# Kernel optimization log

Hardware: AMD Instinct MI355X
Metric: run time of the kernel (lower is better)

The kernel has to match this reference:

```python
import jax, jax.numpy as jnp
import numpy as np

EMBED_DIM = 1024
NUM_HEADS = 16
HEAD_DIM = EMBED_DIM // NUM_HEADS
B, S = 2, 2048


def setup_inputs() -> dict:
    key = jax.random.key(0)
    ks = jax.random.split(key, 11)
    scale = 1.0 / np.sqrt(EMBED_DIM)
    inp = {
        "q": jax.random.normal(ks[0], (B, S, EMBED_DIM), jnp.float32),
        "k": jax.random.normal(ks[1], (B, S, EMBED_DIM), jnp.float32),
        "v": jax.random.normal(ks[2], (B, S, EMBED_DIM), jnp.float32),
        "Wq": jax.random.normal(ks[3], (EMBED_DIM, EMBED_DIM), jnp.float32) * scale,
        "bq": jnp.zeros((EMBED_DIM,), jnp.float32),
        "Wk": jax.random.normal(ks[4], (EMBED_DIM, EMBED_DIM), jnp.float32) * scale,
        "bk": jnp.zeros((EMBED_DIM,), jnp.float32),
        "Wv": jax.random.normal(ks[5], (EMBED_DIM, EMBED_DIM), jnp.float32) * scale,
        "bv": jnp.zeros((EMBED_DIM,), jnp.float32),
        "Wo": jax.random.normal(ks[6], (EMBED_DIM, EMBED_DIM), jnp.float32) * scale,
        "bo": jnp.zeros((EMBED_DIM,), jnp.float32),
    }
    return inp


def _split_heads(x):
    # [B, S, E] -> [B, H, S, D]
    b, s, _ = x.shape
    return x.reshape(b, s, NUM_HEADS, HEAD_DIM).transpose(0, 2, 1, 3)


def reference(q, k, v, Wq, bq, Wk, bk, Wv, bv, Wo, bo):
    query = _split_heads(q @ Wq + bq)  # [B,H,S,D]
    key_ = _split_heads(k @ Wk + bk)
    value = _split_heads(v @ Wv + bv)
    # scaled dot-product attention (scale by sqrt(head_dim), as in source)
    logits = jnp.einsum("bhqd,bhkd->bhqk", query, key_) / jnp.sqrt(
        jnp.asarray(HEAD_DIM, jnp.float32)
    )
    weights = jax.nn.softmax(logits, axis=-1)
    attn = jnp.einsum("bhqk,bhkd->bhqd", weights, value)  # [B,H,S,D]
    concat = attn.transpose(0, 2, 1, 3).reshape(q.shape[0], -1, EMBED_DIM)
    return concat @ Wo + bo
```

## Files before the change

### kernel.cpp

```cpp
#include <hip/hip_runtime.h>
#include <hip/hip_bf16.h>
#include <math.h>


typedef short bf16x8 __attribute__((ext_vector_type(8)));
typedef short bf16x4 __attribute__((ext_vector_type(4)));
typedef float f32x4 __attribute__((ext_vector_type(4)));
typedef unsigned short u16;
typedef unsigned int u32;

#if defined(__HIP_DEVICE_COMPILE__) && __has_builtin(__builtin_amdgcn_mfma_f32_16x16x16_bf16)
#define MFMA16(a, b, c) __builtin_amdgcn_mfma_f32_16x16x16_bf16(a, b, c, 0, 0, 0)
#else
#define MFMA16(a, b, c) __builtin_amdgcn_mfma_f32_16x16x16bf16_1k(a, b, c, 0, 0, 0)
#endif

#define QSCALE 0.18033688011112042f

__device__ __forceinline__ u16 f2b(float f) {
  union { float f; unsigned u; } v; v.f = f;
  unsigned r = v.u + 0x7FFF + ((v.u >> 16) & 1);
  return (u16)(r >> 16);
}

__device__ __forceinline__ void glds16(const u16* g, u16* l) {
  __builtin_amdgcn_global_load_lds(
      (const __attribute__((address_space(1))) u32*)g,
      (__attribute__((address_space(3))) u32*)l, 16, 0, 0);
}

__global__ void prep(const float* __restrict__ q, const float* __restrict__ k,
                     const float* __restrict__ v, u16* __restrict__ qo,
                     u16* __restrict__ ko, u16* __restrict__ vo,
                     const float* __restrict__ W0, const float* __restrict__ W1,
                     const float* __restrict__ W2, const float* __restrict__ W3,
                     u16* __restrict__ T0, u16* __restrict__ T1,
                     u16* __restrict__ T2, u16* __restrict__ T3) {
  __shared__ float tile[64][65];
  int z = blockIdx.y;
  if (z < 3) {
    const float* in = z == 0 ? q : (z == 1 ? k : v);
    u16* out = z == 0 ? qo : (z == 1 ? ko : vo);
    int i = (blockIdx.x * 256 + threadIdx.x) * 8;
    float4 a = *(const float4*)(in + i);
    float4 b = *(const float4*)(in + i + 4);
    union { u16 u[8]; uint4 v4; } o;
    o.u[0] = f2b(a.x); o.u[1] = f2b(a.y); o.u[2] = f2b(a.z); o.u[3] = f2b(a.w);
    o.u[4] = f2b(b.x); o.u[5] = f2b(b.y); o.u[6] = f2b(b.z); o.u[7] = f2b(b.w);
    *(uint4*)(out + i) = o.v4;
  } else {
    int bx = blockIdx.x;
    if (bx >= 1024) return;
    int wsel = bx >> 8, tid2 = bx & 255;
    const float* W = wsel == 0 ? W0 : (wsel == 1 ? W1 : (wsel == 2 ? W2 : W3));
    u16* WT = wsel == 0 ? T0 : (wsel == 1 ? T1 : (wsel == 2 ? T2 : T3));
    int k0 = (tid2 >> 4) * 64, n0 = (tid2 & 15) * 64;
    int c = threadIdx.x & 63, r0 = threadIdx.x >> 6;
    #pragma unroll
    for (int i = 0; i < 64; i += 4)
      tile[r0 + i][c] = W[(k0 + r0 + i) * 1024 + n0 + c];
    __syncthreads();
    #pragma unroll
    for (int i = 0; i < 64; i += 4)
      WT[(n0 + r0 + i) * 1024 + k0 + c] = f2b(tile[c][r0 + i]);
  }
}

template<int MODE, int BM, int BN>
__device__ __forceinline__ void gemm_core(
    const u16* __restrict__ A, const u16* __restrict__ BT,
    const float* __restrict__ bias, void* __restrict__ out,
    int bx, int by, float scale, u16* As, u16* Bs) {
  constexpr int MT = BM / 32;
  constexpr int NT = BN / 32;
  const int tid = threadIdx.x;
  const int w = tid >> 6, lane = tid & 63;
  const int wm = w >> 1, wn = w & 1;
  const int q = lane >> 4, l16 = lane & 15;
  const int m0 = by * BM, n0 = bx * BN;
  const int K = 1024;

  f32x4 acc[MT][NT] = {};
  for (int k0 = 0; k0 < K; k0 += 64) {
    __syncthreads();
    #pragma unroll
    for (int p = 0; p < BM / 32; ++p) {
      int c = p * 4 + w;
      int ci = c * 64 + lane;
      int r = ci >> 3, b = ci & 7;
      glds16(A + (m0 + r) * K + k0 + ((b ^ (r & 7)) * 8), As + c * 512);
    }
    #pragma unroll
    for (int p = 0; p < BN / 32; ++p) {
      int c = p * 4 + w;
      int ci = c * 64 + lane;
      int r = ci >> 3, b = ci & 7;
      glds16(BT + (n0 + r) * K + k0 + ((b ^ (r & 7)) * 8), Bs + c * 512);
    }
    __builtin_amdgcn_s_waitcnt(0xF70);
    __syncthreads();
    #pragma unroll
    for (int ks = 0; ks < 2; ++ks) {
      bf16x8 af[MT], bf[NT];
      #pragma unroll
      for (int mt = 0; mt < MT; ++mt) {
        int row = wm * (BM / 2) + mt * 16 + l16;
        af[mt] = *(const bf16x8*)(As + row * 64 + (((ks * 4 + q) ^ (row & 7)) * 8));
      }
      #pragma unroll
      for (int nt = 0; nt < NT; ++nt) {
        int row = wn * (BN / 2) + nt * 16 + l16;
        bf[nt] = *(const bf16x8*)(Bs + row * 64 + (((ks * 4 + q) ^ (row & 7)) * 8));
      }
      #pragma unroll
      for (int mt = 0; mt < MT; ++mt)
        #pragma unroll
        for (int nt = 0; nt < NT; ++nt)
          acc[mt][nt] = __builtin_amdgcn_mfma_f32_16x16x32_bf16(af[mt], bf[nt], acc[mt][nt], 0, 0, 0);
    }
  }
  #pragma unroll
  for (int mt = 0; mt < MT; ++mt)
    #pragma unroll
    for (int nt = 0; nt < NT; ++nt) {
      int col = n0 + wn * (BN / 2) + nt * 16 + l16;
      float bcol = bias[col];
      if (MODE == 2) {
        int rbase = m0 + wm * (BM / 2) + mt * 16 + q * 4;
        int b = rbase >> 11, s0 = rbase & 2047;
        int h = col >> 6, d = col & 63;
        union { u16 u[4]; uint2 v; } o;
        #pragma unroll
        for (int reg = 0; reg < 4; ++reg)
          o.u[reg] = f2b(acc[mt][nt][reg] + bcol);
        *(uint2*)((u16*)out + (((b << 4) + h) * 64 + d) * 2048 + s0) = o.v;
      } else {
        #pragma unroll
        for (int reg = 0; reg < 4; ++reg) {
          int row = m0 + wm * (BM / 2) + mt * 16 + q * 4 + reg;
          float val = (acc[mt][nt][reg] + bcol) * scale;
          if (MODE == 0) {
            int b = row >> 11, s = row & 2047, h = col >> 6, d = col & 63;
            ((u16*)out)[(((b << 4) + h) * 2048 + s) * 64 + d] = f2b(val);
          } else {
            ((float*)out)[row * 1024 + col] = val;
          }
        }
      }
    }
}

__global__ __launch_bounds__(256) void gemm_qkv(
    const u16* qb, const u16* kb, const u16* vb,
    const u16* WqT, const u16* WkT, const u16* WvT,
    const float* bq, const float* bk, const float* bv,
    u16* Qh, u16* Kh, u16* VhT) {
  __shared__ __align__(16) u16 smem[64 * 64 + 128 * 64];
  u16* As = smem;
  u16* Bs = smem + 64 * 64;
  int l = blockIdx.y * 8 + blockIdx.x;
  int swz = (l & 7) * 64 + (l >> 3);
  int bx = swz & 7, by = swz >> 3;
  int z = blockIdx.z;
  if (z == 0)      gemm_core<0, 64, 128>(qb, WqT, bq, Qh,  bx, by, QSCALE, As, Bs);
  else if (z == 1) gemm_core<0, 64, 128>(kb, WkT, bk, Kh,  bx, by, 1.0f, As, Bs);
  else             gemm_core<2, 64, 128>(vb, WvT, bv, VhT, bx, by, 1.0f, As, Bs);
}

__global__ __launch_bounds__(256) void gemm_out(
    const u16* A, const u16* BT, const float* bias, float* out) {
  __shared__ __align__(16) u16 smem[64 * 64 + 64 * 64];
  u16* As = smem;
  u16* Bs = smem + 64 * 64;
  int bx0 = blockIdx.x, by0 = blockIdx.y;
  int c = bx0 & 7;
  int j = ((bx0 >> 3) << 6) + by0;
  int bx = j & 15;
  int by = (c << 3) + (j >> 4);
  gemm_core<1, 64, 64>(A, BT, bias, out, bx, by, 1.0f, As, Bs);
}

__global__ __launch_bounds__(512, 4) void flash_attn(
    const u16* __restrict__ Qh, const u16* __restrict__ Kh,
    const u16* __restrict__ VTh, u16* __restrict__ Oo) {
  __shared__ __align__(16) u16 smem[32768];
  const int tid = threadIdx.x, w = tid >> 6, lane = tid & 63;
  const int g = w >> 2, w4 = w & 3;
  const int q = lane >> 4, l16 = lane & 15;
  const int bh = blockIdx.x & 31, qt = blockIdx.x >> 5;
  const u16* Qp = Qh + (bh * 2048 + qt * 128) * 64;
  const u16* Kp = Kh + (bh * 2048 + g * 1024) * 64;
  const u16* Vp = VTh + bh * 64 * 2048 + g * 1024;
  u16* Ksg = smem + g * 8192;
  u16* Vtg = smem + 16384 + g * 8192;

  bf16x8 aq[2][2];
  #pragma unroll
  for (int rb = 0; rb < 2; ++rb)
    #pragma unroll
    for (int ks = 0; ks < 2; ++ks)
      aq[rb][ks] = *(const bf16x8*)(Qp + (w4 * 32 + rb * 16 + l16) * 64 + ks * 32 + q * 8);

  const int sr = (lane & 7) ^ (lane >> 3);
  auto stage = [&](int kt, int buf) {
    #pragma unroll
    for (int p = 0; p < 2; ++p) {
      int c = p * 4 + w4;
      int r = c * 8 + (lane >> 3);
      glds16(Kp + (kt * 64 + r) * 64 + sr * 8, Ksg + buf * 4096 + c * 512);
    }
    #pragma unroll
    for (int p = 0; p < 2; ++p) {
      int c = p * 4 + w4;
      int r = c * 8 + (lane >> 3);
      glds16(Vp + r * 2048 + kt * 64 + sr * 8, Vtg + buf * 4096 + c * 512);
    }
  };
  stage(0, 0);

  f32x4 oacc[4][2] = {};
  float lacc[2] = {0.f, 0.f};

  for (int kt = 0; kt < 16; ++kt) {
    const int buf = kt & 1;
    __builtin_amdgcn_s_waitcnt(0xF70);
    __syncthreads();
    if (kt + 1 < 16) stage(kt + 1, buf ^ 1);

    const u16* KsT = Ksg + buf * 4096;
    const u16* VtT = Vtg + buf * 4096;

    f32x4 st[2][4] = {};
    __builtin_amdgcn_s_setprio(1);
    #pragma unroll
    for (int ks = 0; ks < 2; ++ks) {
      bf16x8 bk[4];
      #pragma unroll
      for (int nt = 0; nt < 4; ++nt) {
        int row = nt * 16 + l16;
        bk[nt] = *(const bf16x8*)(KsT + row * 64 + (((ks * 4 + q) ^ (l16 & 7)) * 8));
      }
      #pragma unroll
      for (int rb = 0; rb < 2; ++rb)
        #pragma unroll
        for (int nt = 0; nt < 4; ++nt)
          st[rb][nt] = __builtin_amdgcn_mfma_f32_16x16x32_bf16(bk[nt], aq[rb][ks], st[rb][nt], 0, 0, 0);
    }
    __builtin_amdgcn_s_setprio(0);

    #pragma unroll
    for (int rb = 0; rb < 2; ++rb)
      #pragma unroll
      for (int nt = 0; nt < 4; ++nt)
        #pragma unroll
        for (int reg = 0; reg < 4; ++reg) {
          float p = __builtin_amdgcn_exp2f(st[rb][nt][reg]);
          lacc[rb] += p;
          st[rb][nt][reg] = p;
        }

    __builtin_amdgcn_s_setprio(1);
    #pragma unroll
    for (int kb = 0; kb < 4; ++kb) {
      bf16x4 pf[2];
      #pragma unroll
      for (int rb = 0; rb < 2; ++rb) {
        union { u32 u[2]; bf16x4 v; } pk;
        pk.u[0] = __builtin_amdgcn_perm(__float_as_uint(st[rb][kb][1]),
                                        __float_as_uint(st[rb][kb][0]), 0x07060302u);
        pk.u[1] = __builtin_amdgcn_perm(__float_as_uint(st[rb][kb][3]),
                                        __float_as_uint(st[rb][kb][2]), 0x07060302u);
        pf[rb] = pk.v;
      }
      #pragma unroll
      for (int ntd = 0; ntd < 4; ++ntd) {
        int row = ntd * 16 + l16;
        int c = kb * 2 + (q >> 1);
        bf16x4 vf = *(const bf16x4*)(VtT + row * 64 + ((c ^ (l16 & 7)) * 8) + (q & 1) * 4);
        #pragma unroll
        for (int rb = 0; rb < 2; ++rb)
          oacc[ntd][rb] = MFMA16(vf, pf[rb], oacc[ntd][rb]);
      }
    }
    __builtin_amdgcn_s_setprio(0);
  }

  __syncthreads();
  float* Ocmb = (float*)smem;
  float* Lcmb = (float*)(smem + 18432);
  const int idx = w4 * 64 + lane;
  if (g == 1) {
    #pragma unroll
    for (int ntd = 0; ntd < 4; ++ntd)
      #pragma unroll
      for (int rb = 0; rb < 2; ++rb)
        *(f32x4*)(Ocmb + idx * 36 + ntd * 8 + rb * 4) = oacc[ntd][rb];
    Lcmb[idx * 2 + 0] = lacc[0];
    Lcmb[idx * 2 + 1] = lacc[1];
  }
  __syncthreads();
  if (g == 0) {
    #pragma unroll
    for (int ntd = 0; ntd < 4; ++ntd)
      #pragma unroll
      for (int rb = 0; rb < 2; ++rb)
        oacc[ntd][rb] += *(const f32x4*)(Ocmb + idx * 36 + ntd * 8 + rb * 4);
    lacc[0] += Lcmb[idx * 2 + 0];
    lacc[1] += Lcmb[idx * 2 + 1];

    const int b = bh >> 4, h = bh & 15;
    #pragma unroll
    for (int rb = 0; rb < 2; ++rb) {
      float s = lacc[rb];
      s += __shfl_xor(s, 16);
      s += __shfl_xor(s, 32);
      float rl = 0.998046875f / s;
      int row = b * 2048 + qt * 128 + w4 * 32 + rb * 16 + l16;
      #pragma unroll
      for (int ntd = 0; ntd < 4; ++ntd) {
        union { u16 u[4]; uint2 v; } o;
        #pragma unroll
        for (int reg = 0; reg < 4; ++reg)
          o.u[reg] = f2b(oacc[ntd][rb][reg] * rl);
        *(uint2*)(Oo + row * 1024 + h * 64 + ntd * 16 + q * 4) = o.v;
      }
    }
  }
}

extern "C" void kernel_launch(void* const* d_in, const int* in_sizes, int n_in,
                              void* d_out, int out_size, void* d_ws, size_t ws_size,
                              hipStream_t stream) {
  const float* q  = (const float*)d_in[0];
  const float* k  = (const float*)d_in[1];
  const float* v  = (const float*)d_in[2];
  const float* Wq = (const float*)d_in[3];
  const float* bq = (const float*)d_in[4];
  const float* Wk = (const float*)d_in[5];
  const float* bk = (const float*)d_in[6];
  const float* Wv = (const float*)d_in[7];
  const float* bv = (const float*)d_in[8];
  const float* Wo = (const float*)d_in[9];
  const float* bo = (const float*)d_in[10];

  char* ws = (char*)d_ws;
  const size_t MB = 1024 * 1024;
  u16* qb  = (u16*)(ws);
  u16* kb  = (u16*)(ws + 8 * MB);
  u16* vb  = (u16*)(ws + 16 * MB);
  u16* WqT = (u16*)(ws + 24 * MB);
  u16* WkT = (u16*)(ws + 26 * MB);
  u16* WvT = (u16*)(ws + 28 * MB);
  u16* WoT = (u16*)(ws + 30 * MB);
  u16* Qh  = (u16*)(ws + 32 * MB);
  u16* Kh  = (u16*)(ws + 40 * MB);
  u16* VhT = (u16*)(ws + 48 * MB);
  u16* Ao  = (u16*)(ws + 56 * MB);

  prep<<<dim3(2048, 4), 256, 0, stream>>>(q, k, v, qb, kb, vb,
                                          Wq, Wk, Wv, Wo, WqT, WkT, WvT, WoT);
  gemm_qkv<<<dim3(8, 64, 3), 256, 0, stream>>>(qb, kb, vb, WqT, WkT, WvT,
                                               bq, bk, bv, Qh, Kh, VhT);
  flash_attn<<<512, 512, 0, stream>>>(Qh, Kh, VhT, Ao);
  gemm_out<<<dim3(16, 64), 256, 0, stream>>>(Ao, WoT, bo, (float*)d_out);
}
```

Measured before the change: 220.2 us.

## Double-buffer GEMM LDS tiles and tree-reduce softmax row sums in attention

```diff
diff --git a/kernel.cpp b/kernel.cpp
--- a/kernel.cpp
+++ b/kernel.cpp
@@ -73,6 +73,8 @@
     int bx, int by, float scale, u16* As, u16* Bs) {
   constexpr int MT = BM / 32;
   constexpr int NT = BN / 32;
+  constexpr int ASZ = BM * 64;
+  constexpr int BSZ = BN * 64;
   const int tid = threadIdx.x;
   const int w = tid >> 6, lane = tid & 63;
   const int wm = w >> 1, wn = w & 1;
@@ -80,37 +82,44 @@
   const int m0 = by * BM, n0 = bx * BN;
   const int K = 1024;
 
-  f32x4 acc[MT][NT] = {};
-  for (int k0 = 0; k0 < K; k0 += 64) {
-    __syncthreads();
+  auto stage = [&](int k0, int buf) {
     #pragma unroll
     for (int p = 0; p < BM / 32; ++p) {
       int c = p * 4 + w;
       int ci = c * 64 + lane;
       int r = ci >> 3, b = ci & 7;
-      glds16(A + (m0 + r) * K + k0 + ((b ^ (r & 7)) * 8), As + c * 512);
+      glds16(A + (m0 + r) * K + k0 + ((b ^ (r & 7)) * 8), As + buf * ASZ + c * 512);
     }
     #pragma unroll
     for (int p = 0; p < BN / 32; ++p) {
       int c = p * 4 + w;
       int ci = c * 64 + lane;
       int r = ci >> 3, b = ci & 7;
-      glds16(BT + (n0 + r) * K + k0 + ((b ^ (r & 7)) * 8), Bs + c * 512);
-    }
+      glds16(BT + (n0 + r) * K + k0 + ((b ^ (r & 7)) * 8), Bs + buf * BSZ + c * 512);
+    }
+  };
+  stage(0, 0);
+
+  f32x4 acc[MT][NT] = {};
+  for (int t = 0; t < 16; ++t) {
+    const int buf = t & 1;
     __builtin_amdgcn_s_waitcnt(0xF70);
     __syncthreads();
+    if (t + 1 < 16) stage((t + 1) * 64, buf ^ 1);
+    const u16* Ab = As + buf * ASZ;
+    const u16* Bb = Bs + buf * BSZ;
     #pragma unroll
     for (int ks = 0; ks < 2; ++ks) {
       bf16x8 af[MT], bf[NT];
       #pragma unroll
       for (int mt = 0; mt < MT; ++mt) {
         int row = wm * (BM / 2) + mt * 16 + l16;
-        af[mt] = *(const bf16x8*)(As + row * 64 + (((ks * 4 + q) ^ (row & 7)) * 8));
+        af[mt] = *(const bf16x8*)(Ab + row * 64 + (((ks * 4 + q) ^ (row & 7)) * 8));
       }
       #pragma unroll
       for (int nt = 0; nt < NT; ++nt) {
         int row = wn * (BN / 2) + nt * 16 + l16;
-        bf[nt] = *(const bf16x8*)(Bs + row * 64 + (((ks * 4 + q) ^ (row & 7)) * 8));
+        bf[nt] = *(const bf16x8*)(Bb + row * 64 + (((ks * 4 + q) ^ (row & 7)) * 8));
       }
       #pragma unroll
       for (int mt = 0; mt < MT; ++mt)
@@ -155,9 +164,9 @@
     const u16* WqT, const u16* WkT, const u16* WvT,
     const float* bq, const float* bk, const float* bv,
     u16* Qh, u16* Kh, u16* VhT) {
-  __shared__ __align__(16) u16 smem[64 * 64 + 128 * 64];
+  __shared__ __align__(16) u16 smem[2 * 64 * 64 + 2 * 128 * 64];
   u16* As = smem;
-  u16* Bs = smem + 64 * 64;
+  u16* Bs = smem + 2 * 64 * 64;
   int l = blockIdx.y * 8 + blockIdx.x;
   int swz = (l & 7) * 64 + (l >> 3);
   int bx = swz & 7, by = swz >> 3;
@@ -169,9 +178,9 @@
 
 __global__ __launch_bounds__(256) void gemm_out(
     const u16* A, const u16* BT, const float* bias, float* out) {
-  __shared__ __align__(16) u16 smem[64 * 64 + 64 * 64];
+  __shared__ __align__(16) u16 smem[2 * 64 * 64 + 2 * 64 * 64];
   u16* As = smem;
-  u16* Bs = smem + 64 * 64;
+  u16* Bs = smem + 2 * 64 * 64;
   int bx0 = blockIdx.x, by0 = blockIdx.y;
   int c = bx0 & 7;
   int j = ((bx0 >> 3) << 6) + by0;
@@ -249,15 +258,20 @@
     __builtin_amdgcn_s_setprio(0);
 
     #pragma unroll
-    for (int rb = 0; rb < 2; ++rb)
-      #pragma unroll
-      for (int nt = 0; nt < 4; ++nt)
-        #pragma unroll
-        for (int reg = 0; reg < 4; ++reg) {
-          float p = __builtin_amdgcn_exp2f(st[rb][nt][reg]);
-          lacc[rb] += p;
-          st[rb][nt][reg] = p;
-        }
+    for (int rb = 0; rb < 2; ++rb) {
+      float part[4];
+      #pragma unroll
+      for (int nt = 0; nt < 4; ++nt) {
+        float p0 = __builtin_amdgcn_exp2f(st[rb][nt][0]);
+        float p1 = __builtin_amdgcn_exp2f(st[rb][nt][1]);
+        float p2 = __builtin_amdgcn_exp2f(st[rb][nt][2]);
+        float p3 = __builtin_amdgcn_exp2f(st[rb][nt][3]);
+        st[rb][nt][0] = p0; st[rb][nt][1] = p1;
+        st[rb][nt][2] = p2; st[rb][nt][3] = p3;
+        part[nt] = (p0 + p1) + (p2 + p3);
+      }
+      lacc[rb] += (part[0] + part[1]) + (part[2] + part[3]);
+    }
 
     __builtin_amdgcn_s_setprio(1);
     #pragma unroll
```

New measurement: 219.9 us. No clear change (-0.1%).
